# Kernel tuning notes

Hardware: AMD Instinct MI355X
Metric: run time of the kernel (lower is better)

## Reference

```python
import jax, jax.numpy as jnp
import numpy as np

GROUP_SIZE = 128

def _dequantize(qweight, wscales, wzeros):
    # qweight: [N, K//2] packed bytes, two uint4 values per byte
    # low nibble = even k index, high nibble = odd k index
    N, Kh = qweight.shape
    K = Kh * 2
    low = qweight & 0xF
    high = (qweight >> 4) & 0xF
    w_int = jnp.stack([low, high], axis=-1).reshape(N, K).astype(jnp.float32)  # [N, K]
    G = K // GROUP_SIZE  # number of groups along K
    w_grp = w_int.reshape(N, G, GROUP_SIZE)
    s = wscales.T.reshape(N, G, 1)   # wscales: [G, N] -> [N, G, 1]
    z = wzeros.T.reshape(N, G, 1)
    return ((w_grp - z) * s).reshape(N, K)  # [N, K] dequantized

def setup_inputs() -> dict:
    key = jax.random.key(0)
    k1, k2, k3, k4, k5 = jax.random.split(key, 5)
    M, K, N = 4096, 4096, 12288
    G = K // GROUP_SIZE
    x = jax.random.normal(k1, (M, K), dtype=jnp.float32)
    qweight = jax.random.randint(k2, (N, K // 2), 0, 256, dtype=jnp.int32)
    wscales = jax.random.uniform(k3, (G, N), dtype=jnp.float32) * 0.05
    wzeros = jax.random.uniform(k4, (G, N), dtype=jnp.float32) * 15.0
    bias = jax.random.normal(k5, (N,), dtype=jnp.float32)
    return {"x": x, "qweight": qweight, "wscales": wscales, "wzeros": wzeros, "bias": bias}

def reference(x, qweight, wscales, wzeros, bias):
    # AWQ W4A16 linear: y = x @ dequant(W)^T + b
    w = _dequantize(qweight, wscales, wzeros)  # [N, K]
    return jnp.einsum('mk,nk->mn', x, w) + bias
```

## Files before the change

### kernel.cpp

```cpp
#include <hip/hip_runtime.h>

#define M_DIM 4096
#define K_DIM 4096
#define N_DIM 12288
#define BM 256
#define BN 128
#define BK 64
#define NT (K_DIM / BK)

typedef __bf16 bf16x8  __attribute__((ext_vector_type(8)));
typedef float  floatx16 __attribute__((ext_vector_type(16)));

__global__ __launch_bounds__(256) void xcast_kernel(const float* __restrict__ x,
                                                    __bf16* __restrict__ xb) {
    int idx = blockIdx.x * 256 + threadIdx.x;
    const float4* xv = (const float4*)x;
    float4 a = xv[idx * 2];
    float4 b = xv[idx * 2 + 1];
    bf16x8 o;
    o[0] = (__bf16)a.x; o[1] = (__bf16)a.y; o[2] = (__bf16)a.z; o[3] = (__bf16)a.w;
    o[4] = (__bf16)b.x; o[5] = (__bf16)b.y; o[6] = (__bf16)b.z; o[7] = (__bf16)b.w;
    ((bf16x8*)xb)[idx] = o;
}

__global__ __launch_bounds__(256, 2) void gemm_kernel(const __bf16* __restrict__ A,
                                                      const int* __restrict__ Q,
                                                      const float* __restrict__ scales,
                                                      const float* __restrict__ zeros,
                                                      const float* __restrict__ bias,
                                                      float* __restrict__ C) {
    __shared__ __bf16 As[BM * BK];
    __shared__ __bf16 Bs[BN * BK];

    const int tid  = threadIdx.x;
    const int wave = tid >> 6;
    const int lane = tid & 63;
    const int l32  = lane & 31;
    const int half = lane >> 5;
    const int wm = (wave >> 1) * 128;
    const int wn = (wave & 1) * 64;

    const int bid = blockIdx.y * 16 + blockIdx.x;
    const int sw  = (bid & 7) * 192 + (bid >> 3);
    const int bm0 = (sw & 15) * BM;
    const int bn0 = (sw >> 4) * BN;

    const int rowInChunk = lane >> 3;
    const int slot       = lane & 7;
    const int gread      = (l32 & 7) ^ (((l32 >> 3) & 3) << 1);

    const int brow = tid >> 1;
    const int hk   = tid & 1;
    const int gr   = (brow & 7) ^ (((brow >> 3) & 3) << 1);
    const int ncol = bn0 + brow;
    const int* qrow = Q + (size_t)ncol * (K_DIM / 2) + hk * 16;
    __bf16* bdst = Bs + brow * 64;

    floatx16 acc[4][2] = {};

    int4 q0 = *(const int4*)(qrow + 0);
    int4 q1 = *(const int4*)(qrow + 4);
    int4 q2 = *(const int4*)(qrow + 8);
    int4 q3 = *(const int4*)(qrow + 12);
    float scur = scales[ncol];
    float zcur = zeros[ncol];

    #define DQW(Q4, J) { bf16x8 o; \
        o[0] = (__bf16)(((float)((Q4).x & 15)        - zcur) * scur); \
        o[1] = (__bf16)(((float)(((Q4).x >> 4) & 15) - zcur) * scur); \
        o[2] = (__bf16)(((float)((Q4).y & 15)        - zcur) * scur); \
        o[3] = (__bf16)(((float)(((Q4).y >> 4) & 15) - zcur) * scur); \
        o[4] = (__bf16)(((float)((Q4).z & 15)        - zcur) * scur); \
        o[5] = (__bf16)(((float)(((Q4).z >> 4) & 15) - zcur) * scur); \
        o[6] = (__bf16)(((float)((Q4).w & 15)        - zcur) * scur); \
        o[7] = (__bf16)(((float)(((Q4).w >> 4) & 15) - zcur) * scur); \
        *(bf16x8*)(bdst + (((hk * 4 + (J)) ^ gr) << 3)) = o; }

    for (int kt = 0; kt < NT; ++kt) {
        const int k0 = kt * BK;
        #pragma unroll
        for (int r = 0; r < 8; ++r) {
            const int chunk = wave * 8 + r;
            const int row   = chunk * 8 + rowInChunk;
            const int kblk  = slot ^ rowInChunk ^ ((r & 3) << 1);
            const __bf16* ga = A + (size_t)(bm0 + row) * K_DIM + k0 + kblk * 8;
            __builtin_amdgcn_global_load_lds(
                (const __attribute__((address_space(1))) void*)ga,
                (__attribute__((address_space(3))) void*)(As + chunk * 512), 16, 0, 0);
        }
        DQW(q0, 0); DQW(q1, 1); DQW(q2, 2); DQW(q3, 3);
        __syncthreads();

        const int kn = (kt + 1) & (NT - 1);
        const int cb = kn * 32;
        q0 = *(const int4*)(qrow + cb + 0);
        q1 = *(const int4*)(qrow + cb + 4);
        q2 = *(const int4*)(qrow + cb + 8);
        q3 = *(const int4*)(qrow + cb + 12);
        scur = scales[(kn >> 1) * N_DIM + ncol];
        zcur = zeros[(kn >> 1) * N_DIM + ncol];

        #pragma unroll
        for (int ks = 0; ks < 4; ++ks) {
            const int blk = ks * 2 + half;
            const int off = (blk ^ gread) << 3;
            bf16x8 af[4], bfr[2];
            #pragma unroll
            for (int i = 0; i < 4; ++i)
                af[i] = *(const bf16x8*)(As + (wm + i * 32 + l32) * BK + off);
            #pragma unroll
            for (int t = 0; t < 2; ++t)
                bfr[t] = *(const bf16x8*)(Bs + (wn + t * 32 + l32) * BK + off);
            #pragma unroll
            for (int mi = 0; mi < 4; ++mi)
                #pragma unroll
                for (int ni = 0; ni < 2; ++ni)
                    acc[mi][ni] = __builtin_amdgcn_mfma_f32_32x32x16_bf16(
                        af[mi], bfr[ni], acc[mi][ni], 0, 0, 0);
        }
        __syncthreads();
    }

    #pragma unroll
    for (int ni = 0; ni < 2; ++ni) {
        const int col = bn0 + wn + ni * 32 + l32;
        const float bv = bias[col];
        #pragma unroll
        for (int mi = 0; mi < 4; ++mi) {
            #pragma unroll
            for (int reg = 0; reg < 16; ++reg) {
                const int row = bm0 + wm + mi * 32 + half * 4 + (reg & 3) + 8 * (reg >> 2);
                C[(size_t)row * N_DIM + col] = acc[mi][ni][reg] + bv;
            }
        }
    }
}

extern "C" void kernel_launch(void* const* d_in, const int* in_sizes, int n_in,
                              void* d_out, int out_size, void* d_ws, size_t ws_size,
                              hipStream_t stream) {
    const float* x      = (const float*)d_in[0];
    const int*   qw     = (const int*)d_in[1];
    const float* scales = (const float*)d_in[2];
    const float* zeros  = (const float*)d_in[3];
    const float* bias   = (const float*)d_in[4];
    float* out = (float*)d_out;

    __bf16* xb = (__bf16*)d_ws;

    xcast_kernel<<<(M_DIM * K_DIM / 8) / 256, 256, 0, stream>>>(x, xb);

    dim3 grid(M_DIM / BM, N_DIM / BN);
    gemm_kernel<<<grid, 256, 0, stream>>>(xb, qw, scales, zeros, bias, out);
}
```

Measured before the change: 746.4 us.

## Double-buffer dequantized weight tile and interleave dequant with MFMA steps

Adds a second LDS buffer for the dequantized B tile, so the next tile's int4 unpack and scale work runs inside the MFMA k-substep loop instead of before the barrier. Weight loads are prefetched two tiles ahead. This aims to hide dequant ALU latency behind matrix ops and shorten the critical path between barriers. In exchange it doubles B LDS use and raises register pressure from two sets of prefetched registers, which could hurt occupancy at 2 blocks per CU.

After: 739.5 us. Within noise of the previous version (-0.9%).

```diff
diff --git a/kernel.cpp b/kernel.cpp
--- a/kernel.cpp
+++ b/kernel.cpp
@@ -30,7 +30,7 @@
                                                       const float* __restrict__ bias,
                                                       float* __restrict__ C) {
     __shared__ __bf16 As[BM * BK];
-    __shared__ __bf16 Bs[BN * BK];
+    __shared__ __bf16 Bs[2][BN * BK];
 
     const int tid  = threadIdx.x;
     const int wave = tid >> 6;
@@ -54,30 +54,42 @@
     const int gr   = (brow & 7) ^ (((brow >> 3) & 3) << 1);
     const int ncol = bn0 + brow;
     const int* qrow = Q + (size_t)ncol * (K_DIM / 2) + hk * 16;
-    __bf16* bdst = Bs + brow * 64;
 
     floatx16 acc[4][2] = {};
 
-    int4 q0 = *(const int4*)(qrow + 0);
-    int4 q1 = *(const int4*)(qrow + 4);
-    int4 q2 = *(const int4*)(qrow + 8);
-    int4 q3 = *(const int4*)(qrow + 12);
-    float scur = scales[ncol];
-    float zcur = zeros[ncol];
+    #define DQW(Q4, J, DST, S, Z) { bf16x8 o; \
+        o[0] = (__bf16)(((float)((Q4).x & 15)        - (Z)) * (S)); \
+        o[1] = (__bf16)(((float)(((Q4).x >> 4) & 15) - (Z)) * (S)); \
+        o[2] = (__bf16)(((float)((Q4).y & 15)        - (Z)) * (S)); \
+        o[3] = (__bf16)(((float)(((Q4).y >> 4) & 15) - (Z)) * (S)); \
+        o[4] = (__bf16)(((float)((Q4).z & 15)        - (Z)) * (S)); \
+        o[5] = (__bf16)(((float)(((Q4).z >> 4) & 15) - (Z)) * (S)); \
+        o[6] = (__bf16)(((float)((Q4).w & 15)        - (Z)) * (S)); \
+        o[7] = (__bf16)(((float)(((Q4).w >> 4) & 15) - (Z)) * (S)); \
+        *(bf16x8*)((DST) + (((hk * 4 + (J)) ^ gr) << 3)) = o; }
 
-    #define DQW(Q4, J) { bf16x8 o; \
-        o[0] = (__bf16)(((float)((Q4).x & 15)        - zcur) * scur); \
-        o[1] = (__bf16)(((float)(((Q4).x >> 4) & 15) - zcur) * scur); \
-        o[2] = (__bf16)(((float)((Q4).y & 15)        - zcur) * scur); \
-        o[3] = (__bf16)(((float)(((Q4).y >> 4) & 15) - zcur) * scur); \
-        o[4] = (__bf16)(((float)((Q4).z & 15)        - zcur) * scur); \
-        o[5] = (__bf16)(((float)(((Q4).z >> 4) & 15) - zcur) * scur); \
-        o[6] = (__bf16)(((float)((Q4).w & 15)        - zcur) * scur); \
-        o[7] = (__bf16)(((float)(((Q4).w >> 4) & 15) - zcur) * scur); \
-        *(bf16x8*)(bdst + (((hk * 4 + (J)) ^ gr) << 3)) = o; }
+    {
+        int4 p0 = *(const int4*)(qrow + 0);
+        int4 p1 = *(const int4*)(qrow + 4);
+        int4 p2 = *(const int4*)(qrow + 8);
+        int4 p3 = *(const int4*)(qrow + 12);
+        float sp = scales[ncol];
+        float zp = zeros[ncol];
+        __bf16* d0 = &Bs[0][brow * 64];
+        DQW(p0, 0, d0, sp, zp); DQW(p1, 1, d0, sp, zp);
+        DQW(p2, 2, d0, sp, zp); DQW(p3, 3, d0, sp, zp);
+    }
+    int4 qc0 = *(const int4*)(qrow + 32);
+    int4 qc1 = *(const int4*)(qrow + 36);
+    int4 qc2 = *(const int4*)(qrow + 40);
+    int4 qc3 = *(const int4*)(qrow + 44);
+    float sc = scales[ncol];
+    float zc = zeros[ncol];
 
     for (int kt = 0; kt < NT; ++kt) {
-        const int k0 = kt * BK;
+        const int cur = kt & 1;
+        const int nxt = cur ^ 1;
+        const int k0  = kt * BK;
         #pragma unroll
         for (int r = 0; r < 8; ++r) {
             const int chunk = wave * 8 + r;
@@ -88,18 +100,18 @@
                 (const __attribute__((address_space(1))) void*)ga,
                 (__attribute__((address_space(3))) void*)(As + chunk * 512), 16, 0, 0);
         }
-        DQW(q0, 0); DQW(q1, 1); DQW(q2, 2); DQW(q3, 3);
         __syncthreads();
 
-        const int kn = (kt + 1) & (NT - 1);
-        const int cb = kn * 32;
-        q0 = *(const int4*)(qrow + cb + 0);
-        q1 = *(const int4*)(qrow + cb + 4);
-        q2 = *(const int4*)(qrow + cb + 8);
-        q3 = *(const int4*)(qrow + cb + 12);
-        scur = scales[(kn >> 1) * N_DIM + ncol];
-        zcur = zeros[(kn >> 1) * N_DIM + ncol];
+        const int kn2 = (kt + 2) & (NT - 1);
+        const int cb  = kn2 * 32;
+        int4 qn0 = *(const int4*)(qrow + cb + 0);
+        int4 qn1 = *(const int4*)(qrow + cb + 4);
+        int4 qn2 = *(const int4*)(qrow + cb + 8);
+        int4 qn3 = *(const int4*)(qrow + cb + 12);
+        float sn = scales[(kn2 >> 1) * N_DIM + ncol];
+        float zn = zeros[(kn2 >> 1) * N_DIM + ncol];
 
+        __bf16* bnx = &Bs[nxt][brow * 64];
         #pragma unroll
         for (int ks = 0; ks < 4; ++ks) {
             const int blk = ks * 2 + half;
@@ -110,7 +122,11 @@
                 af[i] = *(const bf16x8*)(As + (wm + i * 32 + l32) * BK + off);
             #pragma unroll
             for (int t = 0; t < 2; ++t)
-                bfr[t] = *(const bf16x8*)(Bs + (wn + t * 32 + l32) * BK + off);
+                bfr[t] = *(const bf16x8*)(&Bs[cur][0] + (wn + t * 32 + l32) * BK + off);
+            if (ks == 0) DQW(qc0, 0, bnx, sc, zc);
+            if (ks == 1) DQW(qc1, 1, bnx, sc, zc);
+            if (ks == 2) DQW(qc2, 2, bnx, sc, zc);
+            if (ks == 3) DQW(qc3, 3, bnx, sc, zc);
             #pragma unroll
             for (int mi = 0; mi < 4; ++mi)
                 #pragma unroll
@@ -119,6 +135,9 @@
                         af[mi], bfr[ni], acc[mi][ni], 0, 0, 0);
         }
         __syncthreads();
+
+        qc0 = qn0; qc1 = qn1; qc2 = qn2; qc3 = qn3;
+        sc = sn; zc = zn;
     }
 
     #pragma unroll
```
